# Optimization experiments

Hardware: AMD Instinct MI355X
Metric: run time of the kernel (lower is better)

Reference implementation:

```python
import jax, jax.numpy as jnp
import numpy as np

D_MODEL = 2048
N_HEADS = 16
HEAD_DIM = D_MODEL // N_HEADS  # 128
ROPE_THETA = 10000.0
BATCH = 2
SEQ_LEN = 2048  # == window_size -> dense causal SDPA path


def setup_inputs() -> dict:
    key = jax.random.key(0)
    ks = jax.random.split(key, 5)
    scale = 1.0 / np.sqrt(D_MODEL)
    x = jax.random.normal(ks[0], (BATCH, SEQ_LEN, D_MODEL), dtype=jnp.float32)
    # torch nn.Linear weights are stored (out_features, in_features); y = x @ W.T
    Wq = jax.random.normal(ks[1], (D_MODEL, D_MODEL), dtype=jnp.float32) * scale
    Wk = jax.random.normal(ks[2], (D_MODEL, D_MODEL), dtype=jnp.float32) * scale
    Wv = jax.random.normal(ks[3], (D_MODEL, D_MODEL), dtype=jnp.float32) * scale
    Wo = jax.random.normal(ks[4], (D_MODEL, D_MODEL), dtype=jnp.float32) * scale
    return {"x": x, "Wq": Wq, "Wk": Wk, "Wv": Wv, "Wo": Wo}


def _apply_rope(x):
    # x: [B, H, S, HEAD_DIM]; interleaved-pair RoPE, positions 0..S-1
    S = x.shape[2]
    inv_freq = 1.0 / (ROPE_THETA ** (jnp.arange(0, HEAD_DIM, 2, dtype=jnp.float32) / HEAD_DIM))
    t = jnp.arange(S, dtype=jnp.float32)
    freqs = jnp.outer(t, inv_freq)            # [S, HEAD_DIM//2]
    cos = jnp.cos(freqs)
    sin = jnp.sin(freqs)
    x1 = x[..., 0::2]
    x2 = x[..., 1::2]
    rot = jnp.stack([x1 * cos - x2 * sin, x1 * sin + x2 * cos], axis=-1)  # [B,H,S,hd/2,2]
    return rot.reshape(x.shape)


def reference(x, Wq, Wk, Wv, Wo):
    B, S, _ = x.shape
    q = (x @ Wq.T).reshape(B, S, N_HEADS, HEAD_DIM).transpose(0, 2, 1, 3)  # [B,H,S,D]
    k = (x @ Wk.T).reshape(B, S, N_HEADS, HEAD_DIM).transpose(0, 2, 1, 3)
    v = (x @ Wv.T).reshape(B, S, N_HEADS, HEAD_DIM).transpose(0, 2, 1, 3)
    q = _apply_rope(q)
    k = _apply_rope(k)
    scores = jnp.einsum("bhqd,bhkd->bhqk", q, k) / np.sqrt(HEAD_DIM).astype(np.float32)
    causal = jnp.tril(jnp.ones((S, S), dtype=bool))
    scores = jnp.where(causal, scores, -jnp.inf)
    attn = jax.nn.softmax(scores, axis=-1)
    out = jnp.einsum("bhqk,bhkd->bhqd", attn, v)
    out = out.transpose(0, 2, 1, 3).reshape(B, S, N_HEADS * HEAD_DIM)
    return out @ Wo.T
```

## Files before the change

kernel.cpp:

```cpp
#include <hip/hip_runtime.h>
#include <stdint.h>

#define D_MODEL 2048
#define SEQ     2048
#define BATCH   2
#define NHEAD   16
#define HD      128
#define MROWS   (BATCH*SEQ)

typedef short short8 __attribute__((ext_vector_type(8)));
typedef float f32x4  __attribute__((ext_vector_type(4)));

__device__ __forceinline__ unsigned short f2b(float f) {
  unsigned int u = __float_as_uint(f);
  u += 0x7fffu + ((u >> 16) & 1u);
  return (unsigned short)(u >> 16);
}
__device__ __forceinline__ float b2f(unsigned short s) {
  return __uint_as_float(((unsigned int)s) << 16);
}
__device__ __forceinline__ void gll16(const void* g, void* l) {
  __builtin_amdgcn_global_load_lds((const __attribute__((address_space(1))) void*)g,
                                   (__attribute__((address_space(3))) void*)l, 16, 0, 0);
}

__global__ __launch_bounds__(256) void cast_all(
    const float* __restrict__ x,  const float* __restrict__ Wq,
    const float* __restrict__ Wk, const float* __restrict__ Wv,
    const float* __restrict__ Wo, unsigned short* __restrict__ dst)
{
  size_t e = ((size_t)blockIdx.x * 256 + threadIdx.x) * 4;
  const size_t XN = (size_t)MROWS * D_MODEL;
  const size_t WN = (size_t)D_MODEL * D_MODEL;
  const float* src; size_t off;
  if (e < XN) { src = x; off = e; }
  else {
    size_t e2 = e - XN;
    int w = (int)(e2 >> 22);
    off = e2 & (WN - 1);
    src = (w == 0) ? Wq : (w == 1) ? Wk : (w == 2) ? Wv : Wo;
  }
  float4 v = *(const float4*)(src + off);
  ushort4 o;
  o.x = f2b(v.x); o.y = f2b(v.y); o.z = f2b(v.z); o.w = f2b(v.w);
  *(ushort4*)(dst + e) = o;
}

__device__ __forceinline__ void gemm_core(
    const unsigned short* __restrict__ A, const unsigned short* __restrict__ Bw,
    unsigned short* As, unsigned short* Bs, int m0, int n0, int tid,
    f32x4 (&acc)[4][4])
{
  const int K = D_MODEL;
  const int wave = tid >> 6, lane = tid & 63, l15 = lane & 15, quad = lane >> 4;
  const int wr = wave >> 1, wc = wave & 1;

  for (int kt = 0; kt < K; kt += 32) {
    #pragma unroll
    for (int c = 0; c < 2; ++c) {
      int chunk = c * 256 + tid;
      const unsigned short* ga = A  + (size_t)(m0 + (chunk >> 2)) * K + kt + (chunk & 3) * 8;
      const unsigned short* gb = Bw + (size_t)(n0 + (chunk >> 2)) * K + kt + (chunk & 3) * 8;
      gll16(ga, As + (size_t)(c * 256 + wave * 64) * 8);
      gll16(gb, Bs + (size_t)(c * 256 + wave * 64) * 8);
    }
    __syncthreads();
    short8 af[4], bfr[4];
    #pragma unroll
    for (int mi = 0; mi < 4; ++mi)
      af[mi] = *(const short8*)(As + (wr * 64 + mi * 16 + l15) * 32 + quad * 8);
    #pragma unroll
    for (int ni = 0; ni < 4; ++ni)
      bfr[ni] = *(const short8*)(Bs + (wc * 64 + ni * 16 + l15) * 32 + quad * 8);
    #pragma unroll
    for (int mi = 0; mi < 4; ++mi)
      #pragma unroll
      for (int ni = 0; ni < 4; ++ni)
        acc[mi][ni] = __builtin_amdgcn_mfma_f32_16x16x32_bf16(af[mi], bfr[ni], acc[mi][ni], 0, 0, 0);
    __syncthreads();
  }
}

__global__ __launch_bounds__(256) void gemm_qkv(
    const unsigned short* __restrict__ Axb,
    const unsigned short* __restrict__ Wq, const unsigned short* __restrict__ Wk,
    const unsigned short* __restrict__ Wv,
    unsigned short* __restrict__ Qh, unsigned short* __restrict__ Kh,
    unsigned short* __restrict__ Vt)
{
  __shared__ unsigned short As[128 * 32], Bs[128 * 32];
  const int z = blockIdx.z;
  const unsigned short* Bw = (z == 0) ? Wq : (z == 1) ? Wk : Wv;
  const int m0 = blockIdx.y * 128, n0 = blockIdx.x * 128;
  f32x4 acc[4][4];
  #pragma unroll
  for (int i = 0; i < 4; ++i)
    #pragma unroll
    for (int j = 0; j < 4; ++j) acc[i][j] = (f32x4){0.f, 0.f, 0.f, 0.f};
  gemm_core(Axb, Bw, As, Bs, m0, n0, threadIdx.x, acc);

  const int tid = threadIdx.x, wave = tid >> 6, lane = tid & 63;
  const int l15 = lane & 15, quad = lane >> 4, wr = wave >> 1, wc = wave & 1;
  if (z < 2) {
    unsigned short* dst = z ? Kh : Qh;
    #pragma unroll
    for (int mi = 0; mi < 4; ++mi)
      #pragma unroll
      for (int ni = 0; ni < 4; ++ni) {
        int row0 = m0 + wr * 64 + mi * 16 + quad * 4;
        int col  = n0 + wc * 64 + ni * 16 + l15;
        int h = col >> 7, d = col & (HD - 1);
        #pragma unroll
        for (int r = 0; r < 4; ++r) {
          int m = row0 + r; int bb = m >> 11; int s = m & (SEQ - 1);
          dst[((size_t)(bb * NHEAD + h) * SEQ + s) * HD + d] = f2b(acc[mi][ni][r]);
        }
      }
  } else {
    #pragma unroll
    for (int mi = 0; mi < 4; ++mi)
      #pragma unroll
      for (int ni = 0; ni < 4; ++ni) {
        int row0 = m0 + wr * 64 + mi * 16 + quad * 4;
        int col  = n0 + wc * 64 + ni * 16 + l15;
        int h = col >> 7, d = col & (HD - 1);
        int bb = row0 >> 11; int s = row0 & (SEQ - 1);
        ushort4 pk;
        pk.x = f2b(acc[mi][ni][0]); pk.y = f2b(acc[mi][ni][1]);
        pk.z = f2b(acc[mi][ni][2]); pk.w = f2b(acc[mi][ni][3]);
        *(ushort4*)(Vt + ((size_t)(bb * NHEAD + h) * HD + d) * SEQ + s) = pk;
      }
  }
}

__global__ __launch_bounds__(256) void gemm_out(
    const unsigned short* __restrict__ A, const unsigned short* __restrict__ Wo,
    float* __restrict__ C)
{
  __shared__ unsigned short As[128 * 32], Bs[128 * 32];
  const int m0 = blockIdx.y * 128, n0 = blockIdx.x * 128;
  f32x4 acc[4][4];
  #pragma unroll
  for (int i = 0; i < 4; ++i)
    #pragma unroll
    for (int j = 0; j < 4; ++j) acc[i][j] = (f32x4){0.f, 0.f, 0.f, 0.f};
  gemm_core(A, Wo, As, Bs, m0, n0, threadIdx.x, acc);

  const int tid = threadIdx.x, wave = tid >> 6, lane = tid & 63;
  const int l15 = lane & 15, quad = lane >> 4, wr = wave >> 1, wc = wave & 1;
  #pragma unroll
  for (int mi = 0; mi < 4; ++mi)
    #pragma unroll
    for (int ni = 0; ni < 4; ++ni) {
      int row0 = m0 + wr * 64 + mi * 16 + quad * 4;
      int col  = n0 + wc * 64 + ni * 16 + l15;
      #pragma unroll
      for (int r = 0; r < 4; ++r)
        C[(size_t)(row0 + r) * D_MODEL + col] = acc[mi][ni][r];
    }
}

__global__ __launch_bounds__(256) void rope_k(unsigned short* __restrict__ Qh,
                                              unsigned short* __restrict__ Kh)
{
  unsigned short* P = blockIdx.y ? Kh : Qh;
  int rid = blockIdx.x * 4 + (threadIdx.x >> 6);
  int i = threadIdx.x & 63;
  int s = rid & (SEQ - 1);
  size_t base = (size_t)rid * HD + 2 * i;
  float inv = exp2f(-(float)i * (13.287712379549449f / 64.0f));
  float ang = (float)s * inv;
  float sn, cs; sincosf(ang, &sn, &cs);
  unsigned int pk = *(const unsigned int*)(P + base);
  float x1 = b2f((unsigned short)(pk & 0xffffu));
  float x2 = b2f((unsigned short)(pk >> 16));
  unsigned short o0 = f2b(x1 * cs - x2 * sn);
  unsigned short o1 = f2b(x1 * sn + x2 * cs);
  *(unsigned int*)(P + base) = (unsigned int)o0 | ((unsigned int)o1 << 16);
}

__global__ __launch_bounds__(256) void attn_k(
    const unsigned short* __restrict__ Qh, const unsigned short* __restrict__ Kh,
    const unsigned short* __restrict__ Vt, unsigned short* __restrict__ Aout)
{
  __shared__ unsigned short Ks[64 * 128];
  __shared__ unsigned short Vs[128 * 64];
  __shared__ unsigned short sPb[4][16 * 72];
  const int tid = threadIdx.x;
  const int wave = tid >> 6, lane = tid & 63, l15 = lane & 15, quad = lane >> 4;
  const int bh = blockIdx.y;
  const int b = bh >> 4, h = bh & 15;
  const unsigned short* Qb = Qh + (size_t)bh * SEQ * HD;
  const unsigned short* Kb = Kh + (size_t)bh * SEQ * HD;
  const unsigned short* Vb = Vt + (size_t)bh * HD * SEQ;
  unsigned short* pw = &sPb[wave][0];
  const float scl = 0.08838834764831845f * 1.4426950408889634f;

  #pragma unroll
  for (int half = 0; half < 2; ++half) {
    const int tile = half ? (31 - blockIdx.x) : blockIdx.x;
    const int q0b = tile * 64;
    const int q0w = q0b + wave * 16;
    const int q = q0w + l15;

    short8 qf[4];
    #pragma unroll
    for (int c = 0; c < 4; ++c)
      qf[c] = *(const short8*)(Qb + (size_t)(q0w + l15) * HD + c * 32 + quad * 8);

    f32x4 o[8];
    #pragma unroll
    for (int dj = 0; dj < 8; ++dj) o[dj] = (f32x4){0.f, 0.f, 0.f, 0.f};
    float ms = -1e30f, ls = 0.f;

    const int trips = tile + 1;
    for (int it = 0; it < trips; ++it) {
      const int k0 = it * 64;
      __syncthreads();
      #pragma unroll
      for (int c = 0; c < 4; ++c) {
        int slot = c * 256 + tid;
        int kr = slot >> 4, pch = slot & 15;
        gll16(Kb + (size_t)(k0 + kr) * HD + ((pch ^ (kr & 15)) * 8), Ks + slot * 8);
      }
      #pragma unroll
      for (int c = 0; c < 4; ++c) {
        int slot = c * 256 + tid;
        int vr = slot >> 3, pch = slot & 7;
        gll16(Vb + (size_t)vr * SEQ + k0 + ((pch ^ (vr & 7)) * 8), Vs + slot * 8);
      }
      __syncthreads();

      f32x4 st[4];
      #pragma unroll
      for (int ni = 0; ni < 4; ++ni) st[ni] = (f32x4){0.f, 0.f, 0.f, 0.f};
      #pragma unroll
      for (int ni = 0; ni < 4; ++ni) {
        const int rowb = (ni * 16 + l15) * 128;
        #pragma unroll
        for (int c = 0; c < 4; ++c) {
          short8 kf = *(const short8*)(Ks + rowb + (((c * 4 + quad) ^ l15) * 8));
          st[ni] = __builtin_amdgcn_mfma_f32_16x16x32_bf16(kf, qf[c], st[ni], 0, 0, 0);
        }
      }

      if (k0 + 63 > q0w) {
        #pragma unroll
        for (int ni = 0; ni < 4; ++ni)
          #pragma unroll
          for (int r = 0; r < 4; ++r) {
            int k = k0 + ni * 16 + quad * 4 + r;
            if (k > q) st[ni][r] = -1e30f;
          }
      }

      float lm = -1e30f;
      #pragma unroll
      for (int ni = 0; ni < 4; ++ni)
        #pragma unroll
        for (int r = 0; r < 4; ++r) lm = fmaxf(lm, st[ni][r]);
      lm = fmaxf(lm, __shfl_xor(lm, 16, 64));
      lm = fmaxf(lm, __shfl_xor(lm, 32, 64));
      float mn = fmaxf(ms, lm);
      float al = exp2f((ms - mn) * scl);
      ms = mn;
      float nm = mn * scl;
      float rs = 0.f;
      #pragma unroll
      for (int ni = 0; ni < 4; ++ni)
        #pragma unroll
        for (int r = 0; r < 4; ++r) {
          float p = exp2f(fmaf(st[ni][r], scl, -nm));
          st[ni][r] = p;
          rs += p;
        }
      rs += __shfl_xor(rs, 16, 64);
      rs += __shfl_xor(rs, 32, 64);
      ls = ls * al + rs;
      #pragma unroll
      for (int dj = 0; dj < 8; ++dj) o[dj] *= al;

      #pragma unroll
      for (int ni = 0; ni < 4; ++ni) {
        ushort4 pk;
        pk.x = f2b(st[ni][0]); pk.y = f2b(st[ni][1]);
        pk.z = f2b(st[ni][2]); pk.w = f2b(st[ni][3]);
        *(ushort4*)(pw + l15 * 72 + ni * 16 + quad * 4) = pk;
      }
      short8 pf0 = *(const short8*)(pw + l15 * 72 + quad * 8);
      short8 pf1 = *(const short8*)(pw + l15 * 72 + 32 + quad * 8);

      #pragma unroll
      for (int dj = 0; dj < 8; ++dj) {
        const int vrow = (dj * 16 + l15) * 64;
        short8 v0 = *(const short8*)(Vs + vrow + (((quad) ^ (l15 & 7)) * 8));
        short8 v1 = *(const short8*)(Vs + vrow + (((4 + quad) ^ (l15 & 7)) * 8));
        o[dj] = __builtin_amdgcn_mfma_f32_16x16x32_bf16(v0, pf0, o[dj], 0, 0, 0);
        o[dj] = __builtin_amdgcn_mfma_f32_16x16x32_bf16(v1, pf1, o[dj], 0, 0, 0);
      }
    }

    float rl = 1.0f / ls;
    #pragma unroll
    for (int dj = 0; dj < 8; ++dj) {
      ushort4 pk;
      pk.x = f2b(o[dj][0] * rl); pk.y = f2b(o[dj][1] * rl);
      pk.z = f2b(o[dj][2] * rl); pk.w = f2b(o[dj][3] * rl);
      *(ushort4*)(Aout + ((size_t)(b * SEQ + q)) * D_MODEL + h * HD + dj * 16 + quad * 4) = pk;
    }
  }
}

extern "C" void kernel_launch(void* const* d_in, const int* in_sizes, int n_in,
                              void* d_out, int out_size, void* d_ws, size_t ws_size,
                              hipStream_t stream)
{
  const float* x  = (const float*)d_in[0];
  const float* Wq = (const float*)d_in[1];
  const float* Wk = (const float*)d_in[2];
  const float* Wv = (const float*)d_in[3];
  const float* Wo = (const float*)d_in[4];
  float* out = (float*)d_out;

  unsigned short* xb  = (unsigned short*)d_ws;
  unsigned short* wqb = xb  + 8388608;
  unsigned short* wkb = wqb + 4194304;
  unsigned short* wvb = wkb + 4194304;
  unsigned short* wob = wvb + 4194304;
  unsigned short* qh  = wob + 4194304;
  unsigned short* kh  = qh  + 8388608;
  unsigned short* vt  = kh  + 8388608;
  unsigned short* ao  = vt  + 8388608;

  cast_all<<<24576, 256, 0, stream>>>(x, Wq, Wk, Wv, Wo, xb);
  gemm_qkv<<<dim3(16, 32, 3), 256, 0, stream>>>(xb, wqb, wkb, wvb, qh, kh, vt);
  rope_k<<<dim3(16384, 2), 256, 0, stream>>>(qh, kh);
  attn_k<<<dim3(16, 32), 256, 0, stream>>>(qh, kh, vt, ao);
  gemm_out<<<dim3(16, 32), 256, 0, stream>>>(ao, wob, out);
}
```

Measured before the change: 430.2 us.

## Use 32x32 MFMA with 128-row query tiles in attention and swizzle GEMM LDS

Result: slower. 487.1 us (+13.2%).

```diff
diff --git a/kernel.cpp b/kernel.cpp
--- a/kernel.cpp
+++ b/kernel.cpp
@@ -10,6 +10,7 @@
 
 typedef short short8 __attribute__((ext_vector_type(8)));
 typedef float f32x4  __attribute__((ext_vector_type(4)));
+typedef float f32x16 __attribute__((ext_vector_type(16)));
 
 __device__ __forceinline__ unsigned short f2b(float f) {
   unsigned int u = __float_as_uint(f);
@@ -59,19 +60,22 @@
     #pragma unroll
     for (int c = 0; c < 2; ++c) {
       int chunk = c * 256 + tid;
-      const unsigned short* ga = A  + (size_t)(m0 + (chunk >> 2)) * K + kt + (chunk & 3) * 8;
-      const unsigned short* gb = Bw + (size_t)(n0 + (chunk >> 2)) * K + kt + (chunk & 3) * 8;
+      int row = chunk >> 2, pch = chunk & 3;
+      int sch = pch ^ ((row >> 1) & 3);
+      const unsigned short* ga = A  + (size_t)(m0 + row) * K + kt + sch * 8;
+      const unsigned short* gb = Bw + (size_t)(n0 + row) * K + kt + sch * 8;
       gll16(ga, As + (size_t)(c * 256 + wave * 64) * 8);
       gll16(gb, Bs + (size_t)(c * 256 + wave * 64) * 8);
     }
     __syncthreads();
+    const int rch = quad ^ ((l15 >> 1) & 3);
     short8 af[4], bfr[4];
     #pragma unroll
     for (int mi = 0; mi < 4; ++mi)
-      af[mi] = *(const short8*)(As + (wr * 64 + mi * 16 + l15) * 32 + quad * 8);
+      af[mi] = *(const short8*)(As + (wr * 64 + mi * 16 + l15) * 32 + rch * 8);
     #pragma unroll
     for (int ni = 0; ni < 4; ++ni)
-      bfr[ni] = *(const short8*)(Bs + (wc * 64 + ni * 16 + l15) * 32 + quad * 8);
+      bfr[ni] = *(const short8*)(Bs + (wc * 64 + ni * 16 + l15) * 32 + rch * 8);
     #pragma unroll
     for (int mi = 0; mi < 4; ++mi)
       #pragma unroll
@@ -185,9 +189,10 @@
 {
   __shared__ unsigned short Ks[64 * 128];
   __shared__ unsigned short Vs[128 * 64];
-  __shared__ unsigned short sPb[4][16 * 72];
+  __shared__ unsigned short sPb[4][32 * 72];
   const int tid = threadIdx.x;
-  const int wave = tid >> 6, lane = tid & 63, l15 = lane & 15, quad = lane >> 4;
+  const int wave = tid >> 6, lane = tid & 63;
+  const int l31 = lane & 31, hf = lane >> 5;
   const int bh = blockIdx.y;
   const int b = bh >> 4, h = bh & 15;
   const unsigned short* Qb = Qh + (size_t)bh * SEQ * HD;
@@ -196,119 +201,129 @@
   unsigned short* pw = &sPb[wave][0];
   const float scl = 0.08838834764831845f * 1.4426950408889634f;
 
-  #pragma unroll
-  for (int half = 0; half < 2; ++half) {
-    const int tile = half ? (31 - blockIdx.x) : blockIdx.x;
-    const int q0b = tile * 64;
-    const int q0w = q0b + wave * 16;
-    const int q = q0w + l15;
-
-    short8 qf[4];
-    #pragma unroll
-    for (int c = 0; c < 4; ++c)
-      qf[c] = *(const short8*)(Qb + (size_t)(q0w + l15) * HD + c * 32 + quad * 8);
-
-    f32x4 o[8];
-    #pragma unroll
-    for (int dj = 0; dj < 8; ++dj) o[dj] = (f32x4){0.f, 0.f, 0.f, 0.f};
-    float ms = -1e30f, ls = 0.f;
-
-    const int trips = tile + 1;
-    for (int it = 0; it < trips; ++it) {
-      const int k0 = it * 64;
-      __syncthreads();
-      #pragma unroll
-      for (int c = 0; c < 4; ++c) {
-        int slot = c * 256 + tid;
-        int kr = slot >> 4, pch = slot & 15;
-        gll16(Kb + (size_t)(k0 + kr) * HD + ((pch ^ (kr & 15)) * 8), Ks + slot * 8);
-      }
-      #pragma unroll
-      for (int c = 0; c < 4; ++c) {
-        int slot = c * 256 + tid;
-        int vr = slot >> 3, pch = slot & 7;
-        gll16(Vb + (size_t)vr * SEQ + k0 + ((pch ^ (vr & 7)) * 8), Vs + slot * 8);
-      }
-      __syncthreads();
-
-      f32x4 st[4];
-      #pragma unroll
-      for (int ni = 0; ni < 4; ++ni) st[ni] = (f32x4){0.f, 0.f, 0.f, 0.f};
-      #pragma unroll
-      for (int ni = 0; ni < 4; ++ni) {
-        const int rowb = (ni * 16 + l15) * 128;
+  const int tile = 15 - blockIdx.x;
+  const int q0b = tile * 128;
+  const int q0w = q0b + wave * 32;
+  const int q = q0w + l31;
+
+  short8 qf[8];
+  #pragma unroll
+  for (int ks = 0; ks < 8; ++ks)
+    qf[ks] = *(const short8*)(Qb + (size_t)q * HD + ks * 16 + hf * 8);
+
+  f32x16 o[4];
+  #pragma unroll
+  for (int mi = 0; mi < 4; ++mi)
+    #pragma unroll
+    for (int r = 0; r < 16; ++r) o[mi][r] = 0.f;
+  float ms = -1e30f, ls = 0.f;
+
+  const int trips = 2 * tile + 2;
+  for (int it = 0; it < trips; ++it) {
+    const int k0 = it * 64;
+    __syncthreads();
+    #pragma unroll
+    for (int c = 0; c < 4; ++c) {
+      int slot = c * 256 + tid;
+      int kr = slot >> 4, pch = slot & 15;
+      gll16(Kb + (size_t)(k0 + kr) * HD + ((pch ^ (kr & 15)) * 8), Ks + slot * 8);
+    }
+    #pragma unroll
+    for (int c = 0; c < 4; ++c) {
+      int slot = c * 256 + tid;
+      int vr = slot >> 3, pch = slot & 7;
+      gll16(Vb + (size_t)vr * SEQ + k0 + ((pch ^ (vr & 7)) * 8), Vs + slot * 8);
+    }
+    __syncthreads();
+    if (k0 > q0w + 31) continue;
+
+    f32x16 st[2];
+    #pragma unroll
+    for (int ni = 0; ni < 2; ++ni)
+      #pragma unroll
+      for (int r = 0; r < 16; ++r) st[ni][r] = 0.f;
+    #pragma unroll
+    for (int ni = 0; ni < 2; ++ni) {
+      const int rowb = (ni * 32 + l31) * 128;
+      #pragma unroll
+      for (int ks = 0; ks < 8; ++ks) {
+        short8 kf = *(const short8*)(Ks + rowb + (((ks * 2 + hf) ^ (lane & 15)) * 8));
+        st[ni] = __builtin_amdgcn_mfma_f32_32x32x16_bf16(kf, qf[ks], st[ni], 0, 0, 0);
+      }
+    }
+
+    if (k0 + 63 > q0w) {
+      #pragma unroll
+      for (int ni = 0; ni < 2; ++ni)
         #pragma unroll
-        for (int c = 0; c < 4; ++c) {
-          short8 kf = *(const short8*)(Ks + rowb + (((c * 4 + quad) ^ l15) * 8));
-          st[ni] = __builtin_amdgcn_mfma_f32_16x16x32_bf16(kf, qf[c], st[ni], 0, 0, 0);
+        for (int r = 0; r < 16; ++r) {
+          int k = k0 + ni * 32 + (r & 3) + 8 * (r >> 2) + 4 * hf;
+          if (k > q) st[ni][r] = -1e30f;
         }
-      }
-
-      if (k0 + 63 > q0w) {
-        #pragma unroll
-        for (int ni = 0; ni < 4; ++ni)
-          #pragma unroll
-          for (int r = 0; r < 4; ++r) {
-            int k = k0 + ni * 16 + quad * 4 + r;
-            if (k > q) st[ni][r] = -1e30f;
-          }
-      }
-
-      float lm = -1e30f;
-      #pragma unroll
-      for (int ni = 0; ni < 4; ++ni)
-        #pragma unroll
-        for (int r = 0; r < 4; ++r) lm = fmaxf(lm, st[ni][r]);
-      lm = fmaxf(lm, __shfl_xor(lm, 16, 64));
-      lm = fmaxf(lm, __shfl_xor(lm, 32, 64));
-      float mn = fmaxf(ms, lm);
-      float al = exp2f((ms - mn) * scl);
-      ms = mn;
-      float nm = mn * scl;
-      float rs = 0.f;
-      #pragma unroll
-      for (int ni = 0; ni < 4; ++ni)
-        #pragma unroll
-        for (int r = 0; r < 4; ++r) {
-          float p = exp2f(fmaf(st[ni][r], scl, -nm));
-          st[ni][r] = p;
-          rs += p;
-        }
-      rs += __shfl_xor(rs, 16, 64);
-      rs += __shfl_xor(rs, 32, 64);
-      ls = ls * al + rs;
-      #pragma unroll
-      for (int dj = 0; dj < 8; ++dj) o[dj] *= al;
-
-      #pragma unroll
-      for (int ni = 0; ni < 4; ++ni) {
+    }
+
+    float lm = -1e30f;
+    #pragma unroll
+    for (int ni = 0; ni < 2; ++ni)
+      #pragma unroll
+      for (int r = 0; r < 16; ++r) lm = fmaxf(lm, st[ni][r]);
+    lm = fmaxf(lm, __shfl_xor(lm, 32, 64));
+    float mn = fmaxf(ms, lm);
+    float al = exp2f((ms - mn) * scl);
+    ms = mn;
+    float nm = mn * scl;
+    float rs = 0.f;
+    #pragma unroll
+    for (int ni = 0; ni < 2; ++ni)
+      #pragma unroll
+      for (int r = 0; r < 16; ++r) {
+        float p = exp2f(fmaf(st[ni][r], scl, -nm));
+        st[ni][r] = p;
+        rs += p;
+      }
+    rs += __shfl_xor(rs, 32, 64);
+    ls = ls * al + rs;
+    #pragma unroll
+    for (int mi = 0; mi < 4; ++mi)
+      #pragma unroll
+      for (int r = 0; r < 16; ++r) o[mi][r] *= al;
+
+    #pragma unroll
+    for (int ni = 0; ni < 2; ++ni)
+      #pragma unroll
+      for (int g = 0; g < 4; ++g) {
         ushort4 pk;
-        pk.x = f2b(st[ni][0]); pk.y = f2b(st[ni][1]);
-        pk.z = f2b(st[ni][2]); pk.w = f2b(st[ni][3]);
-        *(ushort4*)(pw + l15 * 72 + ni * 16 + quad * 4) = pk;
-      }
-      short8 pf0 = *(const short8*)(pw + l15 * 72 + quad * 8);
-      short8 pf1 = *(const short8*)(pw + l15 * 72 + 32 + quad * 8);
-
-      #pragma unroll
-      for (int dj = 0; dj < 8; ++dj) {
-        const int vrow = (dj * 16 + l15) * 64;
-        short8 v0 = *(const short8*)(Vs + vrow + (((quad) ^ (l15 & 7)) * 8));
-        short8 v1 = *(const short8*)(Vs + vrow + (((4 + quad) ^ (l15 & 7)) * 8));
-        o[dj] = __builtin_amdgcn_mfma_f32_16x16x32_bf16(v0, pf0, o[dj], 0, 0, 0);
-        o[dj] = __builtin_amdgcn_mfma_f32_16x16x32_bf16(v1, pf1, o[dj], 0, 0, 0);
-      }
-    }
-
-    float rl = 1.0f / ls;
-    #pragma unroll
-    for (int dj = 0; dj < 8; ++dj) {
+        pk.x = f2b(st[ni][4 * g + 0]); pk.y = f2b(st[ni][4 * g + 1]);
+        pk.z = f2b(st[ni][4 * g + 2]); pk.w = f2b(st[ni][4 * g + 3]);
+        *(ushort4*)(pw + l31 * 72 + ni * 32 + g * 8 + hf * 4) = pk;
+      }
+    short8 pf[4];
+    #pragma unroll
+    for (int ks = 0; ks < 4; ++ks)
+      pf[ks] = *(const short8*)(pw + l31 * 72 + ks * 16 + hf * 8);
+
+    #pragma unroll
+    for (int mi = 0; mi < 4; ++mi) {
+      const int vrow = (mi * 32 + l31) * 64;
+      #pragma unroll
+      for (int ks = 0; ks < 4; ++ks) {
+        short8 vf = *(const short8*)(Vs + vrow + (((ks * 2 + hf) ^ (lane & 7)) * 8));
+        o[mi] = __builtin_amdgcn_mfma_f32_32x32x16_bf16(vf, pf[ks], o[mi], 0, 0, 0);
+      }
+    }
+  }
+
+  float rl = 1.0f / ls;
+  #pragma unroll
+  for (int mi = 0; mi < 4; ++mi)
+    #pragma unroll
+    for (int g = 0; g < 4; ++g) {
       ushort4 pk;
-      pk.x = f2b(o[dj][0] * rl); pk.y = f2b(o[dj][1] * rl);
-      pk.z = f2b(o[dj][2] * rl); pk.w = f2b(o[dj][3] * rl);
-      *(ushort4*)(Aout + ((size_t)(b * SEQ + q)) * D_MODEL + h * HD + dj * 16 + quad * 4) = pk;
-    }
-  }
+      pk.x = f2b(o[mi][4 * g + 0] * rl); pk.y = f2b(o[mi][4 * g + 1] * rl);
+      pk.z = f2b(o[mi][4 * g + 2] * rl); pk.w = f2b(o[mi][4 * g + 3] * rl);
+      *(ushort4*)(Aout + ((size_t)(b * SEQ + q)) * D_MODEL + h * HD
+                  + mi * 32 + g * 8 + hf * 4) = pk;
+    }
 }
 
 extern "C" void kernel_launch(void* const* d_in, const int* in_sizes, int n_in,
```

## Swizzle GEMM LDS tiles and load attention K/V directly from global memory

Applied to the files above, without the earlier changes.

Result: slower. 784.1 us (+82.2%).

```diff
diff --git a/kernel.cpp b/kernel.cpp
--- a/kernel.cpp
+++ b/kernel.cpp
@@ -59,19 +59,22 @@
     #pragma unroll
     for (int c = 0; c < 2; ++c) {
       int chunk = c * 256 + tid;
-      const unsigned short* ga = A  + (size_t)(m0 + (chunk >> 2)) * K + kt + (chunk & 3) * 8;
-      const unsigned short* gb = Bw + (size_t)(n0 + (chunk >> 2)) * K + kt + (chunk & 3) * 8;
+      int row = chunk >> 2, pch = chunk & 3;
+      int sch = pch ^ ((row >> 1) & 3);
+      const unsigned short* ga = A  + (size_t)(m0 + row) * K + kt + sch * 8;
+      const unsigned short* gb = Bw + (size_t)(n0 + row) * K + kt + sch * 8;
       gll16(ga, As + (size_t)(c * 256 + wave * 64) * 8);
       gll16(gb, Bs + (size_t)(c * 256 + wave * 64) * 8);
     }
     __syncthreads();
+    const int rch = quad ^ ((l15 >> 1) & 3);
     short8 af[4], bfr[4];
     #pragma unroll
     for (int mi = 0; mi < 4; ++mi)
-      af[mi] = *(const short8*)(As + (wr * 64 + mi * 16 + l15) * 32 + quad * 8);
+      af[mi] = *(const short8*)(As + (wr * 64 + mi * 16 + l15) * 32 + rch * 8);
     #pragma unroll
     for (int ni = 0; ni < 4; ++ni)
-      bfr[ni] = *(const short8*)(Bs + (wc * 64 + ni * 16 + l15) * 32 + quad * 8);
+      bfr[ni] = *(const short8*)(Bs + (wc * 64 + ni * 16 + l15) * 32 + rch * 8);
     #pragma unroll
     for (int mi = 0; mi < 4; ++mi)
       #pragma unroll
@@ -183,9 +186,7 @@
     const unsigned short* __restrict__ Qh, const unsigned short* __restrict__ Kh,
     const unsigned short* __restrict__ Vt, unsigned short* __restrict__ Aout)
 {
-  __shared__ unsigned short Ks[64 * 128];
-  __shared__ unsigned short Vs[128 * 64];
-  __shared__ unsigned short sPb[4][16 * 72];
+  __shared__ unsigned short sPb[4][16 * 88];
   const int tid = threadIdx.x;
   const int wave = tid >> 6, lane = tid & 63, l15 = lane & 15, quad = lane >> 4;
   const int bh = blockIdx.y;
@@ -196,118 +197,100 @@
   unsigned short* pw = &sPb[wave][0];
   const float scl = 0.08838834764831845f * 1.4426950408889634f;
 
-  #pragma unroll
-  for (int half = 0; half < 2; ++half) {
-    const int tile = half ? (31 - blockIdx.x) : blockIdx.x;
-    const int q0b = tile * 64;
-    const int q0w = q0b + wave * 16;
-    const int q = q0w + l15;
-
-    short8 qf[4];
-    #pragma unroll
-    for (int c = 0; c < 4; ++c)
-      qf[c] = *(const short8*)(Qb + (size_t)(q0w + l15) * HD + c * 32 + quad * 8);
-
-    f32x4 o[8];
-    #pragma unroll
-    for (int dj = 0; dj < 8; ++dj) o[dj] = (f32x4){0.f, 0.f, 0.f, 0.f};
-    float ms = -1e30f, ls = 0.f;
-
-    const int trips = tile + 1;
-    for (int it = 0; it < trips; ++it) {
-      const int k0 = it * 64;
-      __syncthreads();
+  const int t16 = 127 - (blockIdx.x * 4 + wave);
+  const int q0w = t16 * 16;
+  const int q = q0w + l15;
+
+  short8 qf[4];
+  #pragma unroll
+  for (int c = 0; c < 4; ++c)
+    qf[c] = *(const short8*)(Qb + (size_t)q * HD + c * 32 + quad * 8);
+
+  f32x4 o[8];
+  #pragma unroll
+  for (int dj = 0; dj < 8; ++dj) o[dj] = (f32x4){0.f, 0.f, 0.f, 0.f};
+  float ms = -1e30f, ls = 0.f;
+
+  const int trips = (q0w >> 6) + 1;
+  for (int it = 0; it < trips; ++it) {
+    const int k0 = it * 64;
+
+    f32x4 st[4];
+    #pragma unroll
+    for (int ni = 0; ni < 4; ++ni) st[ni] = (f32x4){0.f, 0.f, 0.f, 0.f};
+    #pragma unroll
+    for (int ni = 0; ni < 4; ++ni) {
+      const unsigned short* krow = Kb + (size_t)(k0 + ni * 16 + l15) * HD;
       #pragma unroll
       for (int c = 0; c < 4; ++c) {
-        int slot = c * 256 + tid;
-        int kr = slot >> 4, pch = slot & 15;
-        gll16(Kb + (size_t)(k0 + kr) * HD + ((pch ^ (kr & 15)) * 8), Ks + slot * 8);
+        short8 kf = *(const short8*)(krow + c * 32 + quad * 8);
+        st[ni] = __builtin_amdgcn_mfma_f32_16x16x32_bf16(kf, qf[c], st[ni], 0, 0, 0);
       }
-      #pragma unroll
-      for (int c = 0; c < 4; ++c) {
-        int slot = c * 256 + tid;
-        int vr = slot >> 3, pch = slot & 7;
-        gll16(Vb + (size_t)vr * SEQ + k0 + ((pch ^ (vr & 7)) * 8), Vs + slot * 8);
-      }
-      __syncthreads();
-
-      f32x4 st[4];
-      #pragma unroll
-      for (int ni = 0; ni < 4; ++ni) st[ni] = (f32x4){0.f, 0.f, 0.f, 0.f};
-      #pragma unroll
-      for (int ni = 0; ni < 4; ++ni) {
-        const int rowb = (ni * 16 + l15) * 128;
-        #pragma unroll
-        for (int c = 0; c < 4; ++c) {
-          short8 kf = *(const short8*)(Ks + rowb + (((c * 4 + quad) ^ l15) * 8));
-          st[ni] = __builtin_amdgcn_mfma_f32_16x16x32_bf16(kf, qf[c], st[ni], 0, 0, 0);
-        }
-      }
-
-      if (k0 + 63 > q0w) {
-        #pragma unroll
-        for (int ni = 0; ni < 4; ++ni)
-          #pragma unroll
-          for (int r = 0; r < 4; ++r) {
-            int k = k0 + ni * 16 + quad * 4 + r;
-            if (k > q) st[ni][r] = -1e30f;
-          }
-      }
-
-      float lm = -1e30f;
-      #pragma unroll
-      for (int ni = 0; ni < 4; ++ni)
-        #pragma unroll
-        for (int r = 0; r < 4; ++r) lm = fmaxf(lm, st[ni][r]);
-      lm = fmaxf(lm, __shfl_xor(lm, 16, 64));
-      lm = fmaxf(lm, __shfl_xor(lm, 32, 64));
-      float mn = fmaxf(ms, lm);
-      float al = exp2f((ms - mn) * scl);
-      ms = mn;
-      float nm = mn * scl;
-      float rs = 0.f;
+    }
+
+    if (k0 + 63 > q0w) {
       #pragma unroll
       for (int ni = 0; ni < 4; ++ni)
         #pragma unroll
         for (int r = 0; r < 4; ++r) {
-          float p = exp2f(fmaf(st[ni][r], scl, -nm));
-          st[ni][r] = p;
-          rs += p;
+          int k = k0 + ni * 16 + quad * 4 + r;
+          if (k > q) st[ni][r] = -1e30f;
         }
-      rs += __shfl_xor(rs, 16, 64);
-      rs += __shfl_xor(rs, 32, 64);
-      ls = ls * al + rs;
-      #pragma unroll
-      for (int dj = 0; dj < 8; ++dj) o[dj] *= al;
-
-      #pragma unroll
-      for (int ni = 0; ni < 4; ++ni) {
-        ushort4 pk;
-        pk.x = f2b(st[ni][0]); pk.y = f2b(st[ni][1]);
-        pk.z = f2b(st[ni][2]); pk.w = f2b(st[ni][3]);
-        *(ushort4*)(pw + l15 * 72 + ni * 16 + quad * 4) = pk;
+    }
+
+    float lm = -1e30f;
+    #pragma unroll
+    for (int ni = 0; ni < 4; ++ni)
+      #pragma unroll
+      for (int r = 0; r < 4; ++r) lm = fmaxf(lm, st[ni][r]);
+    lm = fmaxf(lm, __shfl_xor(lm, 16, 64));
+    lm = fmaxf(lm, __shfl_xor(lm, 32, 64));
+    float mn = fmaxf(ms, lm);
+    float al = exp2f((ms - mn) * scl);
+    ms = mn;
+    float nm = mn * scl;
+    float rs = 0.f;
+    #pragma unroll
+    for (int ni = 0; ni < 4; ++ni)
+      #pragma unroll
+      for (int r = 0; r < 4; ++r) {
+        float p = exp2f(fmaf(st[ni][r], scl, -nm));
+        st[ni][r] = p;
+        rs += p;
       }
-      short8 pf0 = *(const short8*)(pw + l15 * 72 + quad * 8);
-      short8 pf1 = *(const short8*)(pw + l15 * 72 + 32 + quad * 8);
-
-      #pragma unroll
-      for (int dj = 0; dj < 8; ++dj) {
-        const int vrow = (dj * 16 + l15) * 64;
-        short8 v0 = *(const short8*)(Vs + vrow + (((quad) ^ (l15 & 7)) * 8));
-        short8 v1 = *(const short8*)(Vs + vrow + (((4 + quad) ^ (l15 & 7)) * 8));
-        o[dj] = __builtin_amdgcn_mfma_f32_16x16x32_bf16(v0, pf0, o[dj], 0, 0, 0);
-        o[dj] = __builtin_amdgcn_mfma_f32_16x16x32_bf16(v1, pf1, o[dj], 0, 0, 0);
-      }
-    }
-
-    float rl = 1.0f / ls;
+    rs += __shfl_xor(rs, 16, 64);
+    rs += __shfl_xor(rs, 32, 64);
+    ls = ls * al + rs;
+    #pragma unroll
+    for (int dj = 0; dj < 8; ++dj) o[dj] *= al;
+
+    #pragma unroll
+    for (int ni = 0; ni < 4; ++ni) {
+      ushort4 pk;
+      pk.x = f2b(st[ni][0]); pk.y = f2b(st[ni][1]);
+      pk.z = f2b(st[ni][2]); pk.w = f2b(st[ni][3]);
+      *(ushort4*)(pw + l15 * 88 + ni * 16 + quad * 4) = pk;
+    }
+    short8 pf0 = *(const short8*)(pw + l15 * 88 + quad * 8);
+    short8 pf1 = *(const short8*)(pw + l15 * 88 + 32 + quad * 8);
+
     #pragma unroll
     for (int dj = 0; dj < 8; ++dj) {
-      ushort4 pk;
-      pk.x = f2b(o[dj][0] * rl); pk.y = f2b(o[dj][1] * rl);
-      pk.z = f2b(o[dj][2] * rl); pk.w = f2b(o[dj][3] * rl);
-      *(ushort4*)(Aout + ((size_t)(b * SEQ + q)) * D_MODEL + h * HD + dj * 16 + quad * 4) = pk;
-    }
+      const unsigned short* vrow = Vb + (size_t)(dj * 16 + l15) * SEQ + k0;
+      short8 v0 = *(const short8*)(vrow + quad * 8);
+      short8 v1 = *(const short8*)(vrow + 32 + quad * 8);
+      o[dj] = __builtin_amdgcn_mfma_f32_16x16x32_bf16(v0, pf0, o[dj], 0, 0, 0);
+      o[dj] = __builtin_amdgcn_mfma_f32_16x16x32_bf16(v1, pf1, o[dj], 0, 0, 0);
+    }
+  }
+
+  float rl = 1.0f / ls;
+  #pragma unroll
+  for (int dj = 0; dj < 8; ++dj) {
+    ushort4 pk;
+    pk.x = f2b(o[dj][0] * rl); pk.y = f2b(o[dj][1] * rl);
+    pk.z = f2b(o[dj][2] * rl); pk.w = f2b(o[dj][3] * rl);
+    *(ushort4*)(Aout + ((size_t)(b * SEQ + q)) * D_MODEL + h * HD + dj * 16 + quad * 4) = pk;
   }
 }
 
@@ -335,6 +318,6 @@
   cast_all<<<24576, 256, 0, stream>>>(x, Wq, Wk, Wv, Wo, xb);
   gemm_qkv<<<dim3(16, 32, 3), 256, 0, stream>>>(xb, wqb, wkb, wvb, qh, kh, vt);
   rope_k<<<dim3(16384, 2), 256, 0, stream>>>(qh, kh);
-  attn_k<<<dim3(16, 32), 256, 0, stream>>>(qh, kh, vt, ao);
+  attn_k<<<dim3(32, 32), 256, 0, stream>>>(qh, kh, vt, ao);
   gemm_out<<<dim3(16, 32), 256, 0, stream>>>(ao, wob, out);
 }
```

## Double-buffer K/V tiles in attention kernel to overlap loads with compute

Applied to the files above, without the earlier changes.

New measurement: 441.1 us. 1.03x slower.

```diff
diff --git a/kernel.cpp b/kernel.cpp
--- a/kernel.cpp
+++ b/kernel.cpp
@@ -183,8 +183,8 @@
     const unsigned short* __restrict__ Qh, const unsigned short* __restrict__ Kh,
     const unsigned short* __restrict__ Vt, unsigned short* __restrict__ Aout)
 {
-  __shared__ unsigned short Ks[64 * 128];
-  __shared__ unsigned short Vs[128 * 64];
+  __shared__ unsigned short Ks[2][64 * 128];
+  __shared__ unsigned short Vs[2][128 * 64];
   __shared__ unsigned short sPb[4][16 * 72];
   const int tid = threadIdx.x;
   const int wave = tid >> 6, lane = tid & 63, l15 = lane & 15, quad = lane >> 4;
@@ -196,17 +196,19 @@
   unsigned short* pw = &sPb[wave][0];
   const float scl = 0.08838834764831845f * 1.4426950408889634f;
 
+  const int kslot_r = tid >> 4, kslot_c = tid & 15;
+  const int vslot_r = tid >> 3, vslot_c = tid & 7;
+
   #pragma unroll
   for (int half = 0; half < 2; ++half) {
     const int tile = half ? (31 - blockIdx.x) : blockIdx.x;
-    const int q0b = tile * 64;
-    const int q0w = q0b + wave * 16;
+    const int q0w = tile * 64 + wave * 16;
     const int q = q0w + l15;
 
     short8 qf[4];
     #pragma unroll
     for (int c = 0; c < 4; ++c)
-      qf[c] = *(const short8*)(Qb + (size_t)(q0w + l15) * HD + c * 32 + quad * 8);
+      qf[c] = *(const short8*)(Qb + (size_t)q * HD + c * 32 + quad * 8);
 
     f32x4 o[8];
     #pragma unroll
@@ -214,22 +216,46 @@
     float ms = -1e30f, ls = 0.f;
 
     const int trips = tile + 1;
+
+    __syncthreads();
+    #pragma unroll
+    for (int c = 0; c < 4; ++c) {
+      int slot = c * 256 + tid;
+      int kr = kslot_r + c * 16;
+      gll16(Kb + (size_t)kr * HD + ((kslot_c ^ (kr & 15)) * 8), &Ks[0][0] + slot * 8);
+    }
+    #pragma unroll
+    for (int c = 0; c < 4; ++c) {
+      int slot = c * 256 + tid;
+      int vr = vslot_r + c * 32;
+      gll16(Vb + (size_t)vr * SEQ + ((vslot_c ^ (vr & 7)) * 8), &Vs[0][0] + slot * 8);
+    }
+
     for (int it = 0; it < trips; ++it) {
       const int k0 = it * 64;
+      const int buf = it & 1;
       __syncthreads();
-      #pragma unroll
-      for (int c = 0; c < 4; ++c) {
-        int slot = c * 256 + tid;
-        int kr = slot >> 4, pch = slot & 15;
-        gll16(Kb + (size_t)(k0 + kr) * HD + ((pch ^ (kr & 15)) * 8), Ks + slot * 8);
-      }
-      #pragma unroll
-      for (int c = 0; c < 4; ++c) {
-        int slot = c * 256 + tid;
-        int vr = slot >> 3, pch = slot & 7;
-        gll16(Vb + (size_t)vr * SEQ + k0 + ((pch ^ (vr & 7)) * 8), Vs + slot * 8);
-      }
-      __syncthreads();
+
+      if (it + 1 < trips) {
+        const int kn = k0 + 64;
+        unsigned short* kd = &Ks[buf ^ 1][0];
+        unsigned short* vd = &Vs[buf ^ 1][0];
+        #pragma unroll
+        for (int c = 0; c < 4; ++c) {
+          int slot = c * 256 + tid;
+          int kr = kslot_r + c * 16;
+          gll16(Kb + (size_t)(kn + kr) * HD + ((kslot_c ^ (kr & 15)) * 8), kd + slot * 8);
+        }
+        #pragma unroll
+        for (int c = 0; c < 4; ++c) {
+          int slot = c * 256 + tid;
+          int vr = vslot_r + c * 32;
+          gll16(Vb + (size_t)vr * SEQ + kn + ((vslot_c ^ (vr & 7)) * 8), vd + slot * 8);
+        }
+      }
+
+      const unsigned short* Kt = &Ks[buf][0];
+      const unsigned short* Vtl = &Vs[buf][0];
 
       f32x4 st[4];
       #pragma unroll
@@ -239,7 +265,7 @@
         const int rowb = (ni * 16 + l15) * 128;
         #pragma unroll
         for (int c = 0; c < 4; ++c) {
-          short8 kf = *(const short8*)(Ks + rowb + (((c * 4 + quad) ^ l15) * 8));
+          short8 kf = *(const short8*)(Kt + rowb + (((c * 4 + quad) ^ l15) * 8));
           st[ni] = __builtin_amdgcn_mfma_f32_16x16x32_bf16(kf, qf[c], st[ni], 0, 0, 0);
         }
       }
@@ -293,8 +319,8 @@
       #pragma unroll
       for (int dj = 0; dj < 8; ++dj) {
         const int vrow = (dj * 16 + l15) * 64;
-        short8 v0 = *(const short8*)(Vs + vrow + (((quad) ^ (l15 & 7)) * 8));
-        short8 v1 = *(const short8*)(Vs + vrow + (((4 + quad) ^ (l15 & 7)) * 8));
+        short8 v0 = *(const short8*)(Vtl + vrow + (((quad) ^ (l15 & 7)) * 8));
+        short8 v1 = *(const short8*)(Vtl + vrow + (((4 + quad) ^ (l15 & 7)) * 8));
         o[dj] = __builtin_amdgcn_mfma_f32_16x16x32_bf16(v0, pf0, o[dj], 0, 0, 0);
         o[dj] = __builtin_amdgcn_mfma_f32_16x16x32_bf16(v1, pf1, o[dj], 0, 0, 0);
       }
```
